# Kernel optimization log

Measured on AMD Instinct MI355X. Metric: run time of the kernel, lower is better.

## Reference

```python
import jax, jax.numpy as jnp
import numpy as np

K_SIZE = 3
STRIDE = 1
PAD = 1


def setup_inputs() -> dict:
    key = jax.random.key(0)
    k1, k2 = jax.random.split(key)
    x = jax.random.normal(k1, (32, 32, 128, 128), dtype=jnp.float32)
    # torch param shape: (kernel_size, kernel_size, in_channels, out_channels)
    kernel = jax.random.normal(k2, (3, 3, 32, 64), dtype=jnp.float32)
    return {"x": x, "kernel": kernel}


def reference(x, kernel):
    # Faithful to the original: patches are flattened in (c, ki, kj) order while
    # the kernel is flattened via .view(-1, out) in (ki, kj, c) order. The
    # effective weight seen by the matmul is therefore the raw (K,K,C,O) buffer
    # REINTERPRETED as (C,K,K,O) (a reshape, not a transpose).
    O = kernel.shape[-1]
    C = kernel.shape[2]
    w_eff = kernel.reshape(C, K_SIZE, K_SIZE, O)       # (C, kh, kw, O), same buffer order
    w_oihw = jnp.transpose(w_eff, (3, 0, 1, 2))        # (O, C, kh, kw)
    out = jax.lax.conv_general_dilated(
        x, w_oihw,
        window_strides=(STRIDE, STRIDE),
        padding=[(PAD, PAD), (PAD, PAD)],
        dimension_numbers=("NCHW", "OIHW", "NCHW"),
    )
    return out
```

## Files before the change

kernel.cpp:

```cpp
#include <hip/hip_runtime.h>

typedef __attribute__((ext_vector_type(8))) short   bf16x8;
typedef __attribute__((ext_vector_type(4))) float   f32x4;
typedef __attribute__((ext_vector_type(4))) unsigned int u32x4;

#define HT    8
#define WT    32
#define WSPAN 34
#define NR    10

__device__ __forceinline__ unsigned short f2bf(float f) {
    union { float f; unsigned u; } v; v.f = f;
    unsigned u = v.u;
    u += 0x7FFFu + ((u >> 16) & 1u);
    return (unsigned short)(u >> 16);
}

__global__ __launch_bounds__(256, 4)
void conv3x3_fused(const float* __restrict__ x, const float* __restrict__ wk,
                   float* __restrict__ out) {
    const int hb = blockIdx.x, wq4 = blockIdx.y, n = blockIdx.z;
    const int H0 = hb * HT, W0 = wq4 * WT;
    const int tid  = threadIdx.x;
    const int lane = tid & 63, wid = tid >> 6;
    const int lq = lane >> 4, lr = lane & 15;

    __shared__ u32x4 lds[NR * WSPAN * 4];

    const bool act = (tid < 136);
    const int cb = (tid < 128) ? (tid >> 5) : ((tid - 128) >> 1);
    const int wq = (tid < 128) ? (tid & 31) : (32 + ((tid - 128) & 1));

    auto issue_loads = [&](int rg, float (&dst)[8]) {
        const int wg = W0 - 1 + wq;
        const bool ok = act && ((unsigned)rg < 128u) && ((unsigned)wg < 128u);
        const float* p = x + (((n * 32 + cb * 8) * 128 + rg) * 128 + wg);
        #pragma unroll
        for (int j = 0; j < 8; ++j)
            dst[j] = ok ? p[j * 16384] : 0.0f;
    };
    auto lds_write = [&](int row, const float (&src)[8]) {
        if (!act) return;
        const int f = (wq >> 1) & 3;
        u32x4 pk;
        pk[0] = (unsigned)f2bf(src[0]) | ((unsigned)f2bf(src[1]) << 16);
        pk[1] = (unsigned)f2bf(src[2]) | ((unsigned)f2bf(src[3]) << 16);
        pk[2] = (unsigned)f2bf(src[4]) | ((unsigned)f2bf(src[5]) << 16);
        pk[3] = (unsigned)f2bf(src[6]) | ((unsigned)f2bf(src[7]) << 16);
        lds[(row * WSPAN + wq) * 4 + (cb ^ f)] = pk;
    };
    auto frag_read = [&](int row, int w) -> bf16x8 {
        const int f = (w >> 1) & 3;
        union { u32x4 u; bf16x8 v; } cv;
        cv.u = lds[(row * WSPAN + w) * 4 + (lq ^ f)];
        return cv.v;
    };

    float buf[4][8];
    issue_loads(H0 - 1, buf[0]);
    issue_loads(H0,     buf[1]);
    issue_loads(H0 + 1, buf[2]);
    issue_loads(H0 + 2, buf[3]);

#define STAGE(R)                                                              \
    {                                                                         \
        lds_write((R), buf[(R) & 3]);                                         \
        if ((R) + 4 < NR) issue_loads(H0 + (R) + 3, buf[(R) & 3]);            \
    }
    STAGE(0) STAGE(1) STAGE(2) STAGE(3) STAGE(4)
    STAGE(5) STAGE(6) STAGE(7) STAGE(8) STAGE(9)
#undef STAGE

    bf16x8 wA[9];
    #pragma unroll
    for (int p = 0; p < 9; ++p) {
        const int ki = p / 3, kj = p % 3;
        union { bf16x8 v; unsigned short s[8]; } u;
        #pragma unroll
        for (int j = 0; j < 8; ++j) {
            const int c = lq * 8 + j;
            u.s[j] = f2bf(wk[((c * 3 + ki) * 3 + kj) * 64 + wid * 16 + lr]);
        }
        wA[p] = u.v;
    }

    __syncthreads();

    f32x4 acc[3][2];
    const f32x4 zero = {0.f, 0.f, 0.f, 0.f};
    #pragma unroll
    for (int a = 0; a < 3; ++a)
        #pragma unroll
        for (int pg = 0; pg < 2; ++pg) acc[a][pg] = zero;

    float* obase = out + (((size_t)(n * 64 + wid * 16 + lq * 4) * 128) * 128) + W0 + lr;

#define ROW(RHO)                                                              \
    {                                                                         \
        _Pragma("unroll")                                                     \
        for (int pg = 0; pg < 2; ++pg) {                                      \
            const bf16x8 fb0 = frag_read((RHO), pg * 16 + lr + 0);            \
            const bf16x8 fb1 = frag_read((RHO), pg * 16 + lr + 1);            \
            const bf16x8 fb2 = frag_read((RHO), pg * 16 + lr + 2);            \
            _Pragma("unroll")                                                 \
            for (int ki = 0; ki < 3; ++ki) {                                  \
                if ((RHO) - ki < 0 || (RHO) - ki > HT - 1) continue;          \
                const int a = ((RHO) - ki + 1) % 3;                           \
                acc[a][pg] = __builtin_amdgcn_mfma_f32_16x16x32_bf16(         \
                    wA[ki * 3 + 0], fb0, acc[a][pg], 0, 0, 0);                \
                acc[a][pg] = __builtin_amdgcn_mfma_f32_16x16x32_bf16(         \
                    wA[ki * 3 + 1], fb1, acc[a][pg], 0, 0, 0);                \
                acc[a][pg] = __builtin_amdgcn_mfma_f32_16x16x32_bf16(         \
                    wA[ki * 3 + 2], fb2, acc[a][pg], 0, 0, 0);                \
            }                                                                 \
        }                                                                     \
        if ((RHO) >= 2) {                                                     \
            const int h = H0 + (RHO) - 2;                                     \
            const int a = ((RHO) - 1) % 3;                                    \
            _Pragma("unroll")                                                 \
            for (int pg = 0; pg < 2; ++pg) {                                  \
                _Pragma("unroll")                                             \
                for (int j = 0; j < 4; ++j)                                   \
                    obase[(j * 128 + h) * 128 + pg * 16] = acc[a][pg][j];     \
                acc[a][pg] = zero;                                            \
            }                                                                 \
        }                                                                     \
    }

    ROW(0) ROW(1) ROW(2) ROW(3) ROW(4) ROW(5) ROW(6) ROW(7) ROW(8) ROW(9)
#undef ROW
}

extern "C" void kernel_launch(void* const* d_in, const int* in_sizes, int n_in,
                              void* d_out, int out_size, void* d_ws, size_t ws_size,
                              hipStream_t stream) {
    const float* x  = (const float*)d_in[0];
    const float* wk = (const float*)d_in[1];
    float* out = (float*)d_out;
    dim3 grid(16, 4, 32);
    dim3 block(256);
    conv3x3_fused<<<grid, block, 0, stream>>>(x, wk, out);
}
```

Baseline: 43.67 us.

## Process two images per block and overlap second image loads with first image MFMAs

Each block now handles two batch images, using a doubled LDS buffer. The global loads and bf16 packing for the second image are interleaved with the MFMA compute and stores of the first, which hides load latency inside the block. The bf16 weight fragments are also built once and reused for both images. In exchange the grid is halved to 1024 blocks, LDS per block doubles, and launch bounds drop to 3 blocks per CU, which reduces occupancy.

```diff
diff --git a/kernel.cpp b/kernel.cpp
--- a/kernel.cpp
+++ b/kernel.cpp
@@ -8,6 +8,7 @@
 #define WT    32
 #define WSPAN 34
 #define NR    10
+#define HALF  (NR * WSPAN * 4)
 
 __device__ __forceinline__ unsigned short f2bf(float f) {
     union { float f; unsigned u; } v; v.f = f;
@@ -16,30 +17,31 @@
     return (unsigned short)(u >> 16);
 }
 
-__global__ __launch_bounds__(256, 4)
+__global__ __launch_bounds__(256, 3)
 void conv3x3_fused(const float* __restrict__ x, const float* __restrict__ wk,
                    float* __restrict__ out) {
-    const int hb = blockIdx.x, wq4 = blockIdx.y, n = blockIdx.z;
+    const int hb = blockIdx.x, wq4 = blockIdx.y, nz = blockIdx.z;
+    const int n0 = nz * 2, n1 = nz * 2 + 1;
     const int H0 = hb * HT, W0 = wq4 * WT;
     const int tid  = threadIdx.x;
     const int lane = tid & 63, wid = tid >> 6;
     const int lq = lane >> 4, lr = lane & 15;
 
-    __shared__ u32x4 lds[NR * WSPAN * 4];
+    __shared__ u32x4 lds[2 * HALF];
 
     const bool act = (tid < 136);
     const int cb = (tid < 128) ? (tid >> 5) : ((tid - 128) >> 1);
     const int wq = (tid < 128) ? (tid & 31) : (32 + ((tid - 128) & 1));
 
-    auto issue_loads = [&](int rg, float (&dst)[8]) {
+    auto issue_loads = [&](int rg, int nn, float (&dst)[8]) {
         const int wg = W0 - 1 + wq;
         const bool ok = act && ((unsigned)rg < 128u) && ((unsigned)wg < 128u);
-        const float* p = x + (((n * 32 + cb * 8) * 128 + rg) * 128 + wg);
+        const float* p = x + (((nn * 32 + cb * 8) * 128 + rg) * 128 + wg);
         #pragma unroll
         for (int j = 0; j < 8; ++j)
             dst[j] = ok ? p[j * 16384] : 0.0f;
     };
-    auto lds_write = [&](int row, const float (&src)[8]) {
+    auto lds_write = [&](int half, int row, const float (&src)[8]) {
         if (!act) return;
         const int f = (wq >> 1) & 3;
         u32x4 pk;
@@ -47,29 +49,30 @@
         pk[1] = (unsigned)f2bf(src[2]) | ((unsigned)f2bf(src[3]) << 16);
         pk[2] = (unsigned)f2bf(src[4]) | ((unsigned)f2bf(src[5]) << 16);
         pk[3] = (unsigned)f2bf(src[6]) | ((unsigned)f2bf(src[7]) << 16);
-        lds[(row * WSPAN + wq) * 4 + (cb ^ f)] = pk;
+        lds[half * HALF + (row * WSPAN + wq) * 4 + (cb ^ f)] = pk;
     };
-    auto frag_read = [&](int row, int w) -> bf16x8 {
+    auto frag_read = [&](int half, int row, int w) -> bf16x8 {
         const int f = (w >> 1) & 3;
         union { u32x4 u; bf16x8 v; } cv;
-        cv.u = lds[(row * WSPAN + w) * 4 + (lq ^ f)];
+        cv.u = lds[half * HALF + (row * WSPAN + w) * 4 + (lq ^ f)];
         return cv.v;
     };
 
     float buf[4][8];
-    issue_loads(H0 - 1, buf[0]);
-    issue_loads(H0,     buf[1]);
-    issue_loads(H0 + 1, buf[2]);
-    issue_loads(H0 + 2, buf[3]);
 
-#define STAGE(R)                                                              \
+#define STAGE(HF, R, NN)                                                      \
     {                                                                         \
-        lds_write((R), buf[(R) & 3]);                                         \
-        if ((R) + 4 < NR) issue_loads(H0 + (R) + 3, buf[(R) & 3]);            \
+        lds_write((HF), (R), buf[(R) & 3]);                                   \
+        if ((R) + 4 < NR) issue_loads(H0 + (R) + 3, (NN), buf[(R) & 3]);      \
     }
-    STAGE(0) STAGE(1) STAGE(2) STAGE(3) STAGE(4)
-    STAGE(5) STAGE(6) STAGE(7) STAGE(8) STAGE(9)
-#undef STAGE
+
+    issue_loads(H0 - 1, n0, buf[0]);
+    issue_loads(H0,     n0, buf[1]);
+    issue_loads(H0 + 1, n0, buf[2]);
+    issue_loads(H0 + 2, n0, buf[3]);
+    STAGE(0, 0, n0) STAGE(0, 1, n0) STAGE(0, 2, n0) STAGE(0, 3, n0)
+    STAGE(0, 4, n0) STAGE(0, 5, n0) STAGE(0, 6, n0) STAGE(0, 7, n0)
+    STAGE(0, 8, n0) STAGE(0, 9, n0)
 
     bf16x8 wA[9];
     #pragma unroll
@@ -84,8 +87,6 @@
         wA[p] = u.v;
     }
 
-    __syncthreads();
-
     f32x4 acc[3][2];
     const f32x4 zero = {0.f, 0.f, 0.f, 0.f};
     #pragma unroll
@@ -93,15 +94,16 @@
         #pragma unroll
         for (int pg = 0; pg < 2; ++pg) acc[a][pg] = zero;
 
-    float* obase = out + (((size_t)(n * 64 + wid * 16 + lq * 4) * 128) * 128) + W0 + lr;
+    float* obase0 = out + (((size_t)(n0 * 64 + wid * 16 + lq * 4) * 128) * 128) + W0 + lr;
+    float* obase1 = out + (((size_t)(n1 * 64 + wid * 16 + lq * 4) * 128) * 128) + W0 + lr;
 
-#define ROW(RHO)                                                              \
+#define ROW(HF, RHO, OB)                                                      \
     {                                                                         \
         _Pragma("unroll")                                                     \
         for (int pg = 0; pg < 2; ++pg) {                                      \
-            const bf16x8 fb0 = frag_read((RHO), pg * 16 + lr + 0);            \
-            const bf16x8 fb1 = frag_read((RHO), pg * 16 + lr + 1);            \
-            const bf16x8 fb2 = frag_read((RHO), pg * 16 + lr + 2);            \
+            const bf16x8 fb0 = frag_read((HF), (RHO), pg * 16 + lr + 0);      \
+            const bf16x8 fb1 = frag_read((HF), (RHO), pg * 16 + lr + 1);      \
+            const bf16x8 fb2 = frag_read((HF), (RHO), pg * 16 + lr + 2);      \
             _Pragma("unroll")                                                 \
             for (int ki = 0; ki < 3; ++ki) {                                  \
                 if ((RHO) - ki < 0 || (RHO) - ki > HT - 1) continue;          \
@@ -121,14 +123,37 @@
             for (int pg = 0; pg < 2; ++pg) {                                  \
                 _Pragma("unroll")                                             \
                 for (int j = 0; j < 4; ++j)                                   \
-                    obase[(j * 128 + h) * 128 + pg * 16] = acc[a][pg][j];     \
+                    (OB)[(j * 128 + h) * 128 + pg * 16] = acc[a][pg][j];      \
                 acc[a][pg] = zero;                                            \
             }                                                                 \
         }                                                                     \
     }
 
-    ROW(0) ROW(1) ROW(2) ROW(3) ROW(4) ROW(5) ROW(6) ROW(7) ROW(8) ROW(9)
+    __syncthreads();
+
+    ROW(0, 0, obase0)
+    issue_loads(H0 - 1, n1, buf[0]);
+    issue_loads(H0,     n1, buf[1]);
+    ROW(0, 1, obase0)
+    issue_loads(H0 + 1, n1, buf[2]);
+    issue_loads(H0 + 2, n1, buf[3]);
+    ROW(0, 2, obase0)
+    STAGE(1, 0, n1) ROW(0, 3, obase0)
+    STAGE(1, 1, n1) ROW(0, 4, obase0)
+    STAGE(1, 2, n1) ROW(0, 5, obase0)
+    STAGE(1, 3, n1) ROW(0, 6, obase0)
+    STAGE(1, 4, n1) ROW(0, 7, obase0)
+    STAGE(1, 5, n1) ROW(0, 8, obase0)
+    STAGE(1, 6, n1) ROW(0, 9, obase0)
+    STAGE(1, 7, n1) STAGE(1, 8, n1) STAGE(1, 9, n1)
+
+    __syncthreads();
+
+    ROW(1, 0, obase1) ROW(1, 1, obase1) ROW(1, 2, obase1) ROW(1, 3, obase1)
+    ROW(1, 4, obase1) ROW(1, 5, obase1) ROW(1, 6, obase1) ROW(1, 7, obase1)
+    ROW(1, 8, obase1) ROW(1, 9, obase1)
 #undef ROW
+#undef STAGE
 }
 
 extern "C" void kernel_launch(void* const* d_in, const int* in_sizes, int n_in,
@@ -137,7 +162,7 @@
     const float* x  = (const float*)d_in[0];
     const float* wk = (const float*)d_in[1];
     float* out = (float*)d_out;
-    dim3 grid(16, 4, 32);
+    dim3 grid(16, 4, 16);
     dim3 block(256);
     conv3x3_fused<<<grid, block, 0, stream>>>(x, wk, out);
 }
```

After: 88.23 us. +102.0%, slower.
